# Kernel optimization log

Hardware: AMD Instinct MI355X
Metric: run time of the kernel (lower is better)

## Reference

```python
import jax, jax.numpy as jnp
import numpy as np

B, L, H = 16, 2048, 768
V, D = 30000, 64


def setup_inputs() -> dict:
    key = jax.random.key(0)
    k1, k2, k3, k4 = jax.random.split(key, 4)
    bert_x = jax.random.normal(k1, (B, L, H), dtype=jnp.float32)
    x = jax.random.randint(k2, (B, L), 0, V, dtype=jnp.int64)
    ae = jax.random.normal(k3, (V, D), dtype=jnp.float32)
    w = jax.random.normal(k4, (D, D), dtype=jnp.float32)
    return {"bert_x": bert_x, "x": x, "ae": ae, "w": w}


def reference(bert_x, x, ae, w):
    # E[b,i] = ae[x[b,i]]  -> [B, L, D]
    E = ae[x]
    # fac[b,i,j] = E[b,i] @ w @ E[b,j]   (bilinear pairwise score)
    scores = jnp.einsum('bid,de,bje->bij', E, w, E)
    Lseq = bert_x.shape[1]
    i = jnp.arange(Lseq, dtype=bert_x.dtype)[:, None]
    j = jnp.arange(Lseq, dtype=bert_x.dtype)[None, :]
    # strictly-causal weight (i+1)/(j+1) for i < j, zero elsewhere
    coef = jnp.where(i < j, (i + 1.0) / (j + 1.0), 0.0).astype(bert_x.dtype)
    # res[:, j] = bert_x[:, j] + sum_{i<j} bert_x[:, i] * coef[i,j] * fac[b,i,j]
    res = bert_x + jnp.einsum('bij,bih->bjh', scores * coef, bert_x)
    return res
```

## Files before the change

kernel.cpp:

```cpp
#include <hip/hip_runtime.h>

#define Bb 16
#define Ll 2048
#define Hh 768
#define Dd 64
#define Cc 64
#define HC 64
#define NT (Hh / HC)
#define NCH (Ll / Cc)
#define NPASS (Hh / 64)

typedef __attribute__((ext_vector_type(8))) short bf16x8;
typedef __attribute__((ext_vector_type(4))) float f32x4;

__device__ __forceinline__ short f2bf(float f) {
  union { float f; unsigned u; } c;
  c.f = f;
  unsigned r = (c.u + 0x7FFFu + ((c.u >> 16) & 1u)) >> 16;
  return (short)r;
}
__device__ __forceinline__ unsigned pack2(float a, float b) {
  return (unsigned)(unsigned short)f2bf(a) | ((unsigned)(unsigned short)f2bf(b) << 16);
}
__device__ __forceinline__ float bf2f(unsigned short s) {
  union { unsigned u; float f; } c;
  c.u = ((unsigned)s) << 16;
  return c.f;
}

__device__ __forceinline__ void sync_lds() {
  asm volatile("s_waitcnt lgkmcnt(0)\n\ts_barrier" ::: "memory");
}

__global__ __launch_bounds__(256) void prep_kernel(const int* __restrict__ x,
                                                   const float* __restrict__ ae,
                                                   const float* __restrict__ w,
                                                   const float* __restrict__ bx,
                                                   short* __restrict__ Eg,
                                                   short* __restrict__ scTg,
                                                   short* __restrict__ Sch) {
  const int tid = threadIdx.x;
  const int wv = tid >> 6, lane = tid & 63, quad = lane >> 4, lq = lane & 15;
  const int b = blockIdx.x >> 5, ch = blockIdx.x & 31;
  const size_t gb = (size_t)blockIdx.x * 4096;
  __shared__ short sE[64 * 64];
  __shared__ short sWT[64 * 64];
  __shared__ short sF[64 * 64];
  __shared__ short sFT[64 * 64];
  __shared__ short sGT[2][64 * 64];

  {
    const int i = tid >> 2, seg = tid & 3;
    const int idx = x[b * Ll + ch * Cc + i];
    const float4* aer = (const float4*)(ae + (size_t)idx * Dd) + seg * 4;
    float4 ev[4];
#pragma unroll
    for (int q = 0; q < 4; ++q) ev[q] = aer[q];
    uint4 pA, pB;
    pA.x = pack2(ev[0].x, ev[0].y); pA.y = pack2(ev[0].z, ev[0].w);
    pA.z = pack2(ev[1].x, ev[1].y); pA.w = pack2(ev[1].z, ev[1].w);
    pB.x = pack2(ev[2].x, ev[2].y); pB.y = pack2(ev[2].z, ev[2].w);
    pB.z = pack2(ev[3].x, ev[3].y); pB.w = pack2(ev[3].z, ev[3].w);
    *(uint4*)&sE[i * 64 + (((2 * seg) ^ (i & 7)) << 3)] = pA;
    *(uint4*)&sE[i * 64 + (((2 * seg + 1) ^ (i & 7)) << 3)] = pB;
    *(uint4*)(Eg + gb + i * 64 + seg * 16) = pA;
    *(uint4*)(Eg + gb + i * 64 + seg * 16 + 8) = pB;
    const float4* wr = (const float4*)w;
#pragma unroll
    for (int q = 0; q < 4; ++q) {
      const int fl = q * 256 + tid;
      const int d = fl >> 4, es = (fl & 15) * 4;
      const float4 v = wr[fl];
      const float vv[4] = {v.x, v.y, v.z, v.w};
#pragma unroll
      for (int c = 0; c < 4; ++c) {
        const int e = es + c;
        sWT[e * 64 + (((d >> 3) ^ (e & 7)) << 3) + (d & 7)] = f2bf(vv[c]);
      }
    }
  }
  __syncthreads();

  const int rm = wv * 16 + lq;
  bf16x8 aE[2], aW[2];
#pragma unroll
  for (int ks = 0; ks < 2; ++ks) {
    const int blk = ((ks * 4 + quad) ^ (rm & 7)) << 3;
    aE[ks] = *(const bf16x8*)&sE[rm * 64 + blk];
    aW[ks] = *(const bf16x8*)&sWT[rm * 64 + blk];
  }

#pragma unroll
  for (int nt = 0; nt < 4; ++nt) {
    const int rn = nt * 16 + lq;
    f32x4 accF = {}, accT = {};
#pragma unroll
    for (int ks = 0; ks < 2; ++ks) {
      const int blk = ((ks * 4 + quad) ^ (rn & 7)) << 3;
      const bf16x8 bW = *(const bf16x8*)&sWT[rn * 64 + blk];
      const bf16x8 bE = *(const bf16x8*)&sE[rn * 64 + blk];
      accF = __builtin_amdgcn_mfma_f32_16x16x32_bf16(aE[ks], bW, accF, 0, 0, 0);
      accT = __builtin_amdgcn_mfma_f32_16x16x32_bf16(aW[ks], bE, accT, 0, 0, 0);
    }
#pragma unroll
    for (int r = 0; r < 4; ++r) {
      const int i = wv * 16 + quad * 4 + r;
      const int e = nt * 16 + lq;
      sF[i * 64 + (((e >> 3) ^ (i & 7)) << 3) + (e & 7)] = f2bf(accF[r]);
      const int d2 = wv * 16 + quad * 4 + r;
      const int i2 = nt * 16 + lq;
      sFT[d2 * 64 + (((i2 >> 3) ^ (d2 & 7)) << 3) + (i2 & 7)] = f2bf(accT[r]);
    }
  }
  __syncthreads();

  const int ip = tid & 31, hg = tid >> 5;
  float4 rGa[2], rGb[2];
  auto load_G = [&](int p) {
    const float* xr = bx + ((size_t)(b * Ll) + ch * Cc + 2 * ip) * Hh + p * 64 + hg * 8;
    rGa[0] = *(const float4*)(xr);
    rGa[1] = *(const float4*)(xr + 4);
    rGb[0] = *(const float4*)(xr + Hh);
    rGb[1] = *(const float4*)(xr + Hh + 4);
  };
  load_G(0);

#pragma unroll
  for (int nt = 0; nt < 4; ++nt) {
    const int rn = nt * 16 + lq;
    f32x4 acc = {};
#pragma unroll
    for (int ks = 0; ks < 2; ++ks) {
      const int blk = ((ks * 4 + quad) ^ (rn & 7)) << 3;
      const bf16x8 bF = *(const bf16x8*)&sF[rn * 64 + blk];
      acc = __builtin_amdgcn_mfma_f32_16x16x32_bf16(aE[ks], bF, acc, 0, 0, 0);
    }
#pragma unroll
    for (int r = 0; r < 4; ++r) {
      const int j = wv * 16 + quad * 4 + r;
      const int i = nt * 16 + lq;
      scTg[gb + j * 64 + i] = f2bf(i < j ? acc[r] : 0.f);
    }
  }

  bf16x8 bFT[4][2];
#pragma unroll
  for (int nt = 0; nt < 4; ++nt) {
    const int rn = nt * 16 + lq;
#pragma unroll
    for (int ks = 0; ks < 2; ++ks) {
      const int blk = ((ks * 4 + quad) ^ (rn & 7)) << 3;
      bFT[nt][ks] = *(const bf16x8*)&sFT[rn * 64 + blk];
    }
  }

  short* So = Sch + (size_t)blockIdx.x * (Hh * Dd);
#pragma unroll 2
  for (int p = 0; p < NPASS; ++p) {
    const int cur = p & 1;
    {
      const float s0 = (float)(ch * Cc + 2 * ip + 1), s1 = (float)(ch * Cc + 2 * ip + 2);
      const float A[8] = {rGa[0].x, rGa[0].y, rGa[0].z, rGa[0].w,
                          rGa[1].x, rGa[1].y, rGa[1].z, rGa[1].w};
      const float Bv[8] = {rGb[0].x, rGb[0].y, rGb[0].z, rGb[0].w,
                           rGb[1].x, rGb[1].y, rGb[1].z, rGb[1].w};
#pragma unroll
      for (int e = 0; e < 8; ++e) {
        const int hl = hg * 8 + e;
        const int sa = hl * 64 + (((ip >> 2) ^ (hl & 7)) << 3) + 2 * (ip & 3);
        *(unsigned*)&sGT[cur][sa] = pack2(A[e] * s0, Bv[e] * s1);
      }
    }
    if (p + 1 < NPASS) load_G(p + 1);
    sync_lds();
    bf16x8 aG[2];
#pragma unroll
    for (int ks = 0; ks < 2; ++ks) {
      const int blk = ((ks * 4 + quad) ^ (rm & 7)) << 3;
      aG[ks] = *(const bf16x8*)&sGT[cur][rm * 64 + blk];
    }
#pragma unroll
    for (int nt = 0; nt < 4; ++nt) {
      f32x4 acc = {};
#pragma unroll
      for (int ks = 0; ks < 2; ++ks)
        acc = __builtin_amdgcn_mfma_f32_16x16x32_bf16(aG[ks], bFT[nt][ks], acc, 0, 0, 0);
#pragma unroll
      for (int r = 0; r < 4; ++r) {
        const int h = p * 64 + wv * 16 + quad * 4 + r;
        So[h * 64 + nt * 16 + lq] = f2bf(acc[r]);
      }
    }
  }
}

__global__ __launch_bounds__(256) void prefix_kernel(short* __restrict__ Sch) {
  const int b = blockIdx.x / 48;
  const int v = (blockIdx.x % 48) * 256 + threadIdx.x;
  uint2* base = (uint2*)(Sch + (size_t)b * NCH * (Hh * Dd)) + v;
  const int stride = Hh * Dd / 4;
  uint2 va[NCH];
#pragma unroll
  for (int s = 0; s < NCH; ++s) va[s] = base[s * stride];
  float4 acc = {0.f, 0.f, 0.f, 0.f};
#pragma unroll
  for (int s = 0; s < NCH; ++s) {
    uint2 o;
    o.x = pack2(acc.x, acc.y);
    o.y = pack2(acc.z, acc.w);
    base[s * stride] = o;
    acc.x += bf2f((unsigned short)(va[s].x & 0xffffu));
    acc.y += bf2f((unsigned short)(va[s].x >> 16));
    acc.z += bf2f((unsigned short)(va[s].y & 0xffffu));
    acc.w += bf2f((unsigned short)(va[s].y >> 16));
  }
}

__global__ __launch_bounds__(256) void scan_kernel(const float* __restrict__ bx,
                                                   const short* __restrict__ Eg,
                                                   const short* __restrict__ scTg,
                                                   const short* __restrict__ STg,
                                                   float* __restrict__ out) {
  const int s = blockIdx.x;
  const int tile = s >> 9;
  const int bc = s & 511;
  const int b = bc >> 5, ch = bc & 31;
  const int tid = threadIdx.x;
  const int w = tid >> 6, lane = tid & 63, quad = lane >> 4, lq = lane & 15;
  const int ip = tid & 31, hg = tid >> 5;
  const int rj = w * 16 + lq;

  __shared__ short sGT[64 * 64];

  float4 rGa[2], rGb[2];
  {
    const float* xr = bx + ((size_t)(b * Ll) + ch * Cc + 2 * ip) * Hh + tile * HC + hg * 8;
    rGa[0] = *(const float4*)(xr);
    rGa[1] = *(const float4*)(xr + 4);
    rGb[0] = *(const float4*)(xr + Hh);
    rGb[1] = *(const float4*)(xr + Hh + 4);
  }
  bf16x8 aC1[2], aC2[2];
  {
    const size_t tb = (size_t)bc * 4096;
#pragma unroll
    for (int ks = 0; ks < 2; ++ks) {
      const int o = rj * 64 + (ks * 4 + quad) * 8;
      aC1[ks] = *(const bf16x8*)(scTg + tb + o);
      aC2[ks] = *(const bf16x8*)(Eg + tb + o);
    }
  }
  bf16x8 stF[4][2];
  {
    const short* Sp = STg + (size_t)bc * (Hh * Dd);
#pragma unroll
    for (int ht = 0; ht < 4; ++ht) {
      const int h = tile * HC + ht * 16 + lq;
#pragma unroll
      for (int ks = 0; ks < 2; ++ks)
        stF[ht][ks] = *(const bf16x8*)(Sp + h * 64 + (ks * 4 + quad) * 8);
    }
  }

  {
    const float s0 = (float)(ch * Cc + 2 * ip + 1), s1 = (float)(ch * Cc + 2 * ip + 2);
    const float A[8] = {rGa[0].x, rGa[0].y, rGa[0].z, rGa[0].w,
                        rGa[1].x, rGa[1].y, rGa[1].z, rGa[1].w};
    const float Bv[8] = {rGb[0].x, rGb[0].y, rGb[0].z, rGb[0].w,
                         rGb[1].x, rGb[1].y, rGb[1].z, rGb[1].w};
#pragma unroll
    for (int e = 0; e < 8; ++e) {
      const int hl = hg * 8 + e;
      const int sa = hl * 64 + (((ip >> 2) ^ (hl & 7)) << 3) + 2 * (ip & 3);
      *(unsigned*)&sGT[sa] = pack2(A[e] * s0, Bv[e] * s1);
    }
  }
  sync_lds();

#pragma unroll
  for (int ht = 0; ht < 4; ++ht) {
    const int rh = ht * 16 + lq;
    f32x4 accO = {};
#pragma unroll
    for (int ks = 0; ks < 2; ++ks) {
      const int blk = ((ks * 4 + quad) ^ (rh & 7)) << 3;
      const bf16x8 gv = *(const bf16x8*)&sGT[rh * 64 + blk];
      accO = __builtin_amdgcn_mfma_f32_16x16x32_bf16(aC1[ks], gv, accO, 0, 0, 0);
      accO = __builtin_amdgcn_mfma_f32_16x16x32_bf16(aC2[ks], stF[ht][ks], accO, 0, 0, 0);
    }
#pragma unroll
    for (int r = 0; r < 4; ++r) {
      const int gj = ch * Cc + w * 16 + quad * 4 + r;
      const size_t off = ((size_t)(b * Ll) + gj) * Hh + tile * HC + ht * 16 + lq;
      out[off] = bx[off] + accO[r] * (1.0f / (float)(gj + 1));
    }
  }
}

extern "C" void kernel_launch(void* const* d_in, const int* in_sizes, int n_in,
                              void* d_out, int out_size, void* d_ws, size_t ws_size,
                              hipStream_t stream) {
  (void)in_sizes; (void)n_in; (void)out_size; (void)ws_size;
  const float* bx = (const float*)d_in[0];
  const int* x = (const int*)d_in[1];
  const float* ae = (const float*)d_in[2];
  const float* w = (const float*)d_in[3];
  float* out = (float*)d_out;
  short* Eg = (short*)d_ws;
  short* scTg = Eg + (size_t)512 * 4096;
  short* Sch = scTg + (size_t)512 * 4096;

  prep_kernel<<<Bb * NCH, 256, 0, stream>>>(x, ae, w, bx, Eg, scTg, Sch);
  prefix_kernel<<<Bb * 48, 256, 0, stream>>>(Sch);
  scan_kernel<<<NT * Bb * NCH, 256, 0, stream>>>(bx, Eg, scTg, Sch, out);
}
```

Measured before the change: 265.9 us.

## Fuse per-chunk state computation with prefix sum into a sequential stateprefix kernel

The per-chunk state (G^T·F^T) is no longer computed in prep and scanned by a separate prefix kernel. A new kernel walks all chunks sequentially for each (batch, 32-wide h slice) and accumulates the exclusive prefix state in fp32 registers, writing each prefix once. This removes the bf16 write/read/write round trip of the state and the intermediate bf16 rounding in the prefix sum. The scan kernel now processes 4 h-tiles per block with double-buffered LDS and prefetching, reusing the loaded coefficient fragments. The stateprefix grid is small (384 blocks), and its serial 32-step chain could limit parallelism.

```diff
diff --git a/kernel.cpp b/kernel.cpp
--- a/kernel.cpp
+++ b/kernel.cpp
@@ -8,7 +8,10 @@
 #define HC 64
 #define NT (Hh / HC)
 #define NCH (Ll / Cc)
-#define NPASS (Hh / 64)
+#define TG 4
+#define NTG (NT / TG)
+#define HCs 32
+#define NHS (Hh / HCs)
 
 typedef __attribute__((ext_vector_type(8))) short bf16x8;
 typedef __attribute__((ext_vector_type(4))) float f32x4;
@@ -22,11 +25,6 @@
 __device__ __forceinline__ unsigned pack2(float a, float b) {
   return (unsigned)(unsigned short)f2bf(a) | ((unsigned)(unsigned short)f2bf(b) << 16);
 }
-__device__ __forceinline__ float bf2f(unsigned short s) {
-  union { unsigned u; float f; } c;
-  c.u = ((unsigned)s) << 16;
-  return c.f;
-}
 
 __device__ __forceinline__ void sync_lds() {
   asm volatile("s_waitcnt lgkmcnt(0)\n\ts_barrier" ::: "memory");
@@ -35,10 +33,9 @@
 __global__ __launch_bounds__(256) void prep_kernel(const int* __restrict__ x,
                                                    const float* __restrict__ ae,
                                                    const float* __restrict__ w,
-                                                   const float* __restrict__ bx,
                                                    short* __restrict__ Eg,
-                                                   short* __restrict__ scTg,
-                                                   short* __restrict__ Sch) {
+                                                   short* __restrict__ FTg,
+                                                   short* __restrict__ scTg) {
   const int tid = threadIdx.x;
   const int wv = tid >> 6, lane = tid & 63, quad = lane >> 4, lq = lane & 15;
   const int b = blockIdx.x >> 5, ch = blockIdx.x & 31;
@@ -46,8 +43,6 @@
   __shared__ short sE[64 * 64];
   __shared__ short sWT[64 * 64];
   __shared__ short sF[64 * 64];
-  __shared__ short sFT[64 * 64];
-  __shared__ short sGT[2][64 * 64];
 
   {
     const int i = tid >> 2, seg = tid & 3;
@@ -107,23 +102,12 @@
       const int i = wv * 16 + quad * 4 + r;
       const int e = nt * 16 + lq;
       sF[i * 64 + (((e >> 3) ^ (i & 7)) << 3) + (e & 7)] = f2bf(accF[r]);
-      const int d2 = wv * 16 + quad * 4 + r;
+      const int e2 = wv * 16 + quad * 4 + r;
       const int i2 = nt * 16 + lq;
-      sFT[d2 * 64 + (((i2 >> 3) ^ (d2 & 7)) << 3) + (i2 & 7)] = f2bf(accT[r]);
+      FTg[gb + e2 * 64 + i2] = f2bf(accT[r]);
     }
   }
   __syncthreads();
-
-  const int ip = tid & 31, hg = tid >> 5;
-  float4 rGa[2], rGb[2];
-  auto load_G = [&](int p) {
-    const float* xr = bx + ((size_t)(b * Ll) + ch * Cc + 2 * ip) * Hh + p * 64 + hg * 8;
-    rGa[0] = *(const float4*)(xr);
-    rGa[1] = *(const float4*)(xr + 4);
-    rGb[0] = *(const float4*)(xr + Hh);
-    rGb[1] = *(const float4*)(xr + Hh + 4);
-  };
-  load_G(0);
 
 #pragma unroll
   for (int nt = 0; nt < 4; ++nt) {
@@ -142,77 +126,73 @@
       scTg[gb + j * 64 + i] = f2bf(i < j ? acc[r] : 0.f);
     }
   }
-
-  bf16x8 bFT[4][2];
-#pragma unroll
-  for (int nt = 0; nt < 4; ++nt) {
-    const int rn = nt * 16 + lq;
-#pragma unroll
-    for (int ks = 0; ks < 2; ++ks) {
-      const int blk = ((ks * 4 + quad) ^ (rn & 7)) << 3;
-      bFT[nt][ks] = *(const bf16x8*)&sFT[rn * 64 + blk];
-    }
-  }
-
-  short* So = Sch + (size_t)blockIdx.x * (Hh * Dd);
-#pragma unroll 2
-  for (int p = 0; p < NPASS; ++p) {
-    const int cur = p & 1;
+}
+
+__global__ __launch_bounds__(256) void stateprefix_kernel(const float* __restrict__ bx,
+                                                          const short* __restrict__ FTg,
+                                                          short* __restrict__ STg) {
+  const int id = blockIdx.x;
+  const int b = id & 15, ht = id >> 4;
+  const int tid = threadIdx.x;
+  const int wv = tid >> 6, lane = tid & 63, quad = lane >> 4, lq = lane & 15;
+  const int mh = wv >> 1, nh = wv & 1;
+  const int ip = tid & 31, hg = tid >> 5;
+  const int rm = mh * 16 + lq;
+
+  __shared__ short sGT[2][HCs * 64];
+
+  f32x4 acc[2] = {};
+  float4 rGa, rGb;
+  auto load_G = [&](int ch) {
+    const float* xr = bx + ((size_t)(b * Ll) + ch * Cc + 2 * ip) * Hh + ht * HCs + hg * 4;
+    rGa = *(const float4*)xr;
+    rGb = *(const float4*)(xr + Hh);
+  };
+  load_G(0);
+
+  for (int ch = 0; ch < NCH; ++ch) {
+    const size_t gb = (size_t)(b * NCH + ch) * 4096;
+    bf16x8 bD[2][2];
+#pragma unroll
+    for (int t = 0; t < 2; ++t) {
+      const int rn = (nh * 2 + t) * 16 + lq;
+#pragma unroll
+      for (int ks = 0; ks < 2; ++ks)
+        bD[t][ks] = *(const bf16x8*)(FTg + gb + rn * 64 + (ks * 4 + quad) * 8);
+    }
+    short* gbuf = sGT[ch & 1];
     {
-      const float s0 = (float)(ch * Cc + 2 * ip + 1), s1 = (float)(ch * Cc + 2 * ip + 2);
-      const float A[8] = {rGa[0].x, rGa[0].y, rGa[0].z, rGa[0].w,
-                          rGa[1].x, rGa[1].y, rGa[1].z, rGa[1].w};
-      const float Bv[8] = {rGb[0].x, rGb[0].y, rGb[0].z, rGb[0].w,
-                           rGb[1].x, rGb[1].y, rGb[1].z, rGb[1].w};
-#pragma unroll
-      for (int e = 0; e < 8; ++e) {
-        const int hl = hg * 8 + e;
+      const float s0 = (float)(ch * Cc + 2 * ip + 1), s1 = s0 + 1.0f;
+      const float A[4] = {rGa.x, rGa.y, rGa.z, rGa.w};
+      const float Bv[4] = {rGb.x, rGb.y, rGb.z, rGb.w};
+#pragma unroll
+      for (int e = 0; e < 4; ++e) {
+        const int hl = hg * 4 + e;
         const int sa = hl * 64 + (((ip >> 2) ^ (hl & 7)) << 3) + 2 * (ip & 3);
-        *(unsigned*)&sGT[cur][sa] = pack2(A[e] * s0, Bv[e] * s1);
-      }
-    }
-    if (p + 1 < NPASS) load_G(p + 1);
+        *(unsigned*)&gbuf[sa] = pack2(A[e] * s0, Bv[e] * s1);
+      }
+    }
+    if (ch + 1 < NCH) load_G(ch + 1);
     sync_lds();
+
+    short* So = STg + (size_t)(b * NCH + ch) * (Hh * Dd);
+#pragma unroll
+    for (int t = 0; t < 2; ++t)
+#pragma unroll
+      for (int r = 0; r < 4; ++r) {
+        const int h = ht * HCs + mh * 16 + quad * 4 + r;
+        So[h * 64 + (nh * 2 + t) * 16 + lq] = f2bf(acc[t][r]);
+      }
+
     bf16x8 aG[2];
 #pragma unroll
-    for (int ks = 0; ks < 2; ++ks) {
-      const int blk = ((ks * 4 + quad) ^ (rm & 7)) << 3;
-      aG[ks] = *(const bf16x8*)&sGT[cur][rm * 64 + blk];
-    }
-#pragma unroll
-    for (int nt = 0; nt < 4; ++nt) {
-      f32x4 acc = {};
+    for (int ks = 0; ks < 2; ++ks)
+      aG[ks] = *(const bf16x8*)&gbuf[rm * 64 + (((ks * 4 + quad) ^ (rm & 7)) << 3)];
+#pragma unroll
+    for (int t = 0; t < 2; ++t)
 #pragma unroll
       for (int ks = 0; ks < 2; ++ks)
-        acc = __builtin_amdgcn_mfma_f32_16x16x32_bf16(aG[ks], bFT[nt][ks], acc, 0, 0, 0);
-#pragma unroll
-      for (int r = 0; r < 4; ++r) {
-        const int h = p * 64 + wv * 16 + quad * 4 + r;
-        So[h * 64 + nt * 16 + lq] = f2bf(acc[r]);
-      }
-    }
-  }
-}
-
-__global__ __launch_bounds__(256) void prefix_kernel(short* __restrict__ Sch) {
-  const int b = blockIdx.x / 48;
-  const int v = (blockIdx.x % 48) * 256 + threadIdx.x;
-  uint2* base = (uint2*)(Sch + (size_t)b * NCH * (Hh * Dd)) + v;
-  const int stride = Hh * Dd / 4;
-  uint2 va[NCH];
-#pragma unroll
-  for (int s = 0; s < NCH; ++s) va[s] = base[s * stride];
-  float4 acc = {0.f, 0.f, 0.f, 0.f};
-#pragma unroll
-  for (int s = 0; s < NCH; ++s) {
-    uint2 o;
-    o.x = pack2(acc.x, acc.y);
-    o.y = pack2(acc.z, acc.w);
-    base[s * stride] = o;
-    acc.x += bf2f((unsigned short)(va[s].x & 0xffffu));
-    acc.y += bf2f((unsigned short)(va[s].x >> 16));
-    acc.z += bf2f((unsigned short)(va[s].y & 0xffffu));
-    acc.w += bf2f((unsigned short)(va[s].y >> 16));
+        acc[t] = __builtin_amdgcn_mfma_f32_16x16x32_bf16(aG[ks], bD[t][ks], acc[t], 0, 0, 0);
   }
 }
 
@@ -222,7 +202,7 @@
                                                    const short* __restrict__ STg,
                                                    float* __restrict__ out) {
   const int s = blockIdx.x;
-  const int tile = s >> 9;
+  const int tg = s >> 9;
   const int bc = s & 511;
   const int b = bc >> 5, ch = bc & 31;
   const int tid = threadIdx.x;
@@ -230,70 +210,82 @@
   const int ip = tid & 31, hg = tid >> 5;
   const int rj = w * 16 + lq;
 
-  __shared__ short sGT[64 * 64];
+  __shared__ short sGT[2][64 * 64];
+
+  bf16x8 aC1[2], aC2[2];
+  {
+    const size_t tb = (size_t)bc * 4096;
+#pragma unroll
+    for (int ks = 0; ks < 2; ++ks) {
+      const int o = rj * 64 + (ks * 4 + quad) * 8;
+      aC1[ks] = *(const bf16x8*)(scTg + tb + o);
+      aC2[ks] = *(const bf16x8*)(Eg + tb + o);
+    }
+  }
+  const short* Sp = STg + (size_t)bc * (Hh * Dd);
 
   float4 rGa[2], rGb[2];
-  {
-    const float* xr = bx + ((size_t)(b * Ll) + ch * Cc + 2 * ip) * Hh + tile * HC + hg * 8;
+  bf16x8 stF[4][2];
+  auto load_G = [&](int tl) {
+    const float* xr = bx + ((size_t)(b * Ll) + ch * Cc + 2 * ip) * Hh + tl * HC + hg * 8;
     rGa[0] = *(const float4*)(xr);
     rGa[1] = *(const float4*)(xr + 4);
     rGb[0] = *(const float4*)(xr + Hh);
     rGb[1] = *(const float4*)(xr + Hh + 4);
-  }
-  bf16x8 aC1[2], aC2[2];
-  {
-    const size_t tb = (size_t)bc * 4096;
-#pragma unroll
-    for (int ks = 0; ks < 2; ++ks) {
-      const int o = rj * 64 + (ks * 4 + quad) * 8;
-      aC1[ks] = *(const bf16x8*)(scTg + tb + o);
-      aC2[ks] = *(const bf16x8*)(Eg + tb + o);
-    }
-  }
-  bf16x8 stF[4][2];
-  {
-    const short* Sp = STg + (size_t)bc * (Hh * Dd);
+  };
+  auto load_S = [&](int tl) {
 #pragma unroll
     for (int ht = 0; ht < 4; ++ht) {
-      const int h = tile * HC + ht * 16 + lq;
+      const int h = tl * HC + ht * 16 + lq;
 #pragma unroll
       for (int ks = 0; ks < 2; ++ks)
         stF[ht][ks] = *(const bf16x8*)(Sp + h * 64 + (ks * 4 + quad) * 8);
     }
-  }
-
-  {
-    const float s0 = (float)(ch * Cc + 2 * ip + 1), s1 = (float)(ch * Cc + 2 * ip + 2);
-    const float A[8] = {rGa[0].x, rGa[0].y, rGa[0].z, rGa[0].w,
-                        rGa[1].x, rGa[1].y, rGa[1].z, rGa[1].w};
-    const float Bv[8] = {rGb[0].x, rGb[0].y, rGb[0].z, rGb[0].w,
-                         rGb[1].x, rGb[1].y, rGb[1].z, rGb[1].w};
-#pragma unroll
-    for (int e = 0; e < 8; ++e) {
-      const int hl = hg * 8 + e;
-      const int sa = hl * 64 + (((ip >> 2) ^ (hl & 7)) << 3) + 2 * (ip & 3);
-      *(unsigned*)&sGT[sa] = pack2(A[e] * s0, Bv[e] * s1);
-    }
-  }
-  sync_lds();
-
-#pragma unroll
-  for (int ht = 0; ht < 4; ++ht) {
-    const int rh = ht * 16 + lq;
-    f32x4 accO = {};
-#pragma unroll
-    for (int ks = 0; ks < 2; ++ks) {
-      const int blk = ((ks * 4 + quad) ^ (rh & 7)) << 3;
-      const bf16x8 gv = *(const bf16x8*)&sGT[rh * 64 + blk];
-      accO = __builtin_amdgcn_mfma_f32_16x16x32_bf16(aC1[ks], gv, accO, 0, 0, 0);
-      accO = __builtin_amdgcn_mfma_f32_16x16x32_bf16(aC2[ks], stF[ht][ks], accO, 0, 0, 0);
-    }
-#pragma unroll
-    for (int r = 0; r < 4; ++r) {
-      const int gj = ch * Cc + w * 16 + quad * 4 + r;
-      const size_t off = ((size_t)(b * Ll) + gj) * Hh + tile * HC + ht * 16 + lq;
-      out[off] = bx[off] + accO[r] * (1.0f / (float)(gj + 1));
-    }
+  };
+
+  load_G(tg * TG);
+  load_S(tg * TG);
+
+  const float s0 = (float)(ch * Cc + 2 * ip + 1), s1 = (float)(ch * Cc + 2 * ip + 2);
+
+#pragma unroll
+  for (int t = 0; t < TG; ++t) {
+    const int tl = tg * TG + t;
+    short* gbuf = sGT[t & 1];
+    {
+      const float A[8] = {rGa[0].x, rGa[0].y, rGa[0].z, rGa[0].w,
+                          rGa[1].x, rGa[1].y, rGa[1].z, rGa[1].w};
+      const float Bv[8] = {rGb[0].x, rGb[0].y, rGb[0].z, rGb[0].w,
+                           rGb[1].x, rGb[1].y, rGb[1].z, rGb[1].w};
+#pragma unroll
+      for (int e = 0; e < 8; ++e) {
+        const int hl = hg * 8 + e;
+        const int sa = hl * 64 + (((ip >> 2) ^ (hl & 7)) << 3) + 2 * (ip & 3);
+        *(unsigned*)&gbuf[sa] = pack2(A[e] * s0, Bv[e] * s1);
+      }
+    }
+    if (t + 1 < TG) load_G(tl + 1);
+    sync_lds();
+
+#pragma unroll
+    for (int ht = 0; ht < 4; ++ht) {
+      const int rh = ht * 16 + lq;
+      f32x4 accO = {};
+#pragma unroll
+      for (int ks = 0; ks < 2; ++ks) {
+        const int blk = ((ks * 4 + quad) ^ (rh & 7)) << 3;
+        const bf16x8 gv = *(const bf16x8*)&gbuf[rh * 64 + blk];
+        accO = __builtin_amdgcn_mfma_f32_16x16x32_bf16(aC1[ks], gv, accO, 0, 0, 0);
+        accO = __builtin_amdgcn_mfma_f32_16x16x32_bf16(aC2[ks], stF[ht][ks], accO, 0, 0, 0);
+      }
+#pragma unroll
+      for (int r = 0; r < 4; ++r) {
+        const int gj = ch * Cc + w * 16 + quad * 4 + r;
+        const size_t off = ((size_t)(b * Ll) + gj) * Hh + tl * HC + ht * 16 + lq;
+        out[off] = bx[off] + accO[r] * (1.0f / (float)(gj + 1));
+      }
+    }
+    if (t + 1 < TG) load_S(tl + 1);
   }
 }
 
@@ -307,10 +299,11 @@
   const float* w = (const float*)d_in[3];
   float* out = (float*)d_out;
   short* Eg = (short*)d_ws;
-  short* scTg = Eg + (size_t)512 * 4096;
-  short* Sch = scTg + (size_t)512 * 4096;
-
-  prep_kernel<<<Bb * NCH, 256, 0, stream>>>(x, ae, w, bx, Eg, scTg, Sch);
-  prefix_kernel<<<Bb * 48, 256, 0, stream>>>(Sch);
-  scan_kernel<<<NT * Bb * NCH, 256, 0, stream>>>(bx, Eg, scTg, Sch, out);
-}
+  short* FTg = Eg + (size_t)512 * 4096;
+  short* scTg = FTg + (size_t)512 * 4096;
+  short* STg = scTg + (size_t)512 * 4096;
+
+  prep_kernel<<<Bb * NCH, 256, 0, stream>>>(x, ae, w, Eg, FTg, scTg);
+  stateprefix_kernel<<<NHS * Bb, 256, 0, stream>>>(bx, FTg, STg);
+  scan_kernel<<<NTG * Bb * NCH, 256, 0, stream>>>(bx, Eg, scTg, STg, out);
+}
```

Measured after the change: 275.8 us. 1.04x slower.
